# Optimization experiments

Measured on AMD Instinct MI355X. Metric: run time of the kernel, lower is better.

## Reference

```python
import jax, jax.numpy as jnp
from jax import lax
import numpy as np

N_FFT = 1024
HOP = 256
CUTOFF = N_FFT // 2 + 1  # 513


def _make_bases():
    n = np.arange(N_FFT)
    # periodic hann window (scipy get_window('hann', N, fftbins=True))
    win = 0.5 - 0.5 * np.cos(2.0 * np.pi * n / N_FFT)
    fb = np.fft.fft(np.eye(N_FFT))
    FB = np.vstack([fb[:CUTOFF].real, fb[:CUTOFF].imag])  # [1026, 1024]
    scale = N_FFT / HOP
    fwd = (FB * win[None, :]).astype(np.float32)                      # [1026, 1024]
    inv = (np.linalg.pinv(scale * FB).T * win[None, :]).astype(np.float32)  # [1026, 1024]
    win_sq = (win ** 2).astype(np.float32)
    return jnp.asarray(fwd), jnp.asarray(inv), jnp.asarray(win_sq)

FWD_BASIS, INV_BASIS, WIN_SQ = _make_bases()


def setup_inputs() -> dict:
    key = jax.random.key(0)
    k1, k2 = jax.random.split(key)
    audio = jax.random.normal(k1, (4, 1048576), dtype=jnp.float32)
    bias_spec = jax.random.uniform(k2, (1, CUTOFF, 1), dtype=jnp.float32)
    return {"audio": audio, "bias_spec": bias_spec}


def reference(audio, bias_spec):
    strength = 0.1
    pad = N_FFT // 2
    # ---- STFT.transform: reflect pad + strided conv1d with fourier basis ----
    x = jnp.pad(audio, ((0, 0), (pad, pad)), mode='reflect')[:, None, :]  # [B,1,T+N]
    ft = lax.conv_general_dilated(
        x, FWD_BASIS[:, None, :], window_strides=(HOP,), padding='VALID',
        dimension_numbers=('NCH', 'OIH', 'NCH'))  # [B, 1026, F]
    re, im = ft[:, :CUTOFF, :], ft[:, CUTOFF:, :]
    mag = jnp.sqrt(re * re + im * im)
    phase = jnp.arctan2(im, re)
    # ---- denoise: bias subtract + clamp ----
    mag_d = jnp.maximum(mag - bias_spec * strength, 0.0)
    # ---- STFT.inverse: cos/sin recombine + conv_transpose1d ----
    rec = jnp.concatenate([mag_d * jnp.cos(phase), mag_d * jnp.sin(phase)], axis=1)  # [B,1026,F]
    # conv_transpose1d(stride=HOP) == dilated conv with flipped, channel-swapped kernel
    K = jnp.flip(INV_BASIS, axis=-1)[None, :, :]  # OIH: [1, 1026, 1024]
    inv = lax.conv_general_dilated(
        rec, K, window_strides=(1,), padding=[(N_FFT - 1, N_FFT - 1)],
        lhs_dilation=(HOP,), dimension_numbers=('NCH', 'OIH', 'NCH'))  # [B,1,(F-1)*HOP+N]
    # ---- window_sumsquare (vectorized overlap-add of win_sq) ----
    F = mag.shape[-1]
    n_len = N_FFT + HOP * (F - 1)
    idx = (jnp.arange(F)[:, None] * HOP + jnp.arange(N_FFT)[None, :]).reshape(-1)
    ws = jnp.zeros((n_len,), jnp.float32).at[idx].add(jnp.tile(WIN_SQ, F))
    tiny = jnp.finfo(jnp.float32).tiny
    inv = jnp.where(ws > tiny, inv / ws, inv) * (float(N_FFT) / HOP)
    # trim filter_length/2 from both ends
    return inv[:, :, pad:-pad]
```

## Files before the change

### kernel.cpp

```cpp
#include <hip/hip_runtime.h>
#include <math.h>


#define NFFT 1024
#define HOP  256
#define CUT  513
#define NB   4
#define LAUD 1048576
#define NFR  4097
#define NFRP 4224
#define FTROWS 4232
#define ABLEN 1082368

typedef __attribute__((ext_vector_type(4))) float f32x4;
typedef __attribute__((ext_vector_type(8))) short bf16x8;

#define AS1 __attribute__((address_space(1)))
#define AS3 __attribute__((address_space(3)))

__device__ __forceinline__ unsigned short f2bf(float x) {
    unsigned u = __float_as_uint(x);
    u += 0x7FFF + ((u >> 16) & 1);
    return (unsigned short)(u >> 16);
}

__global__ __launch_bounds__(256) void build_bases_k(
    ushort* __restrict__ fwd, ushort* __restrict__ invW) {
    __shared__ float ctab[1024];
    const int tid = threadIdx.x, bx = blockIdx.x;
    const float CST = 6.135923151542565e-3f;
    #pragma unroll
    for (int i = 0; i < 4; ++i) ctab[(i << 8) + tid] = cosf(CST * (float)((i << 8) + tid));
    __syncthreads();
    #pragma unroll
    for (int r = 0; r < 4; ++r) {
        int c = (bx << 2) + r;
        int k = (c < CUT) ? c : (c - 512);
        #pragma unroll
        for (int ch = 0; ch < 4; ++ch) {
            int n = (ch << 8) + tid;
            int m = (k * n) & 1023;
            float base = (c < CUT) ? ctab[m] : -ctab[(m + 768) & 1023];
            float win = 0.5f - 0.5f * ctab[n];
            fwd[(c << 10) + n] = f2bf(base * win);
        }
    }
    #pragma unroll
    for (int r = 0; r < 4; ++r) {
        int n = (bx << 2) + r;
        float win = 0.5f - 0.5f * ctab[n];
        long obase = ((long)(n & 255) << 12) + ((long)(n >> 8) << 10);
        #pragma unroll
        for (int ch = 0; ch < 4; ++ch) {
            int c = (ch << 8) + tid;
            int k = (c < CUT) ? c : (c - 512);
            int m = (k * n) & 1023;
            float base = (c < CUT) ? ctab[m] : -ctab[(m + 768) & 1023];
            float d = (c == 0 || c == 512) ? (1.0f / 1024.0f) : (2.0f / 1024.0f);
            invW[obase + c] = f2bf(0.25f * base * d * win);
        }
    }
}

__global__ void cvt_audio_k(const float* __restrict__ audio,
                            ushort* __restrict__ aud, ushort* __restrict__ ft) {
    const int NV = ABLEN / 8;
    int idx = blockIdx.x * blockDim.x + threadIdx.x;
    if (idx < NB * NV) {
        int b = idx / NV;
        int t8 = (idx - b * NV) << 3;
        const float* ap = audio + (long)b * LAUD;
        ushort o[8];
        int j0 = t8 - 512;
        if (j0 >= 0 && j0 + 7 < LAUD) {
            f32x4 v0 = *(const f32x4*)(ap + j0);
            f32x4 v1 = *(const f32x4*)(ap + j0 + 4);
            #pragma unroll
            for (int q = 0; q < 4; ++q) { o[q] = f2bf(v0[q]); o[4 + q] = f2bf(v1[q]); }
        } else {
            #pragma unroll
            for (int q = 0; q < 8; ++q) {
                int t = t8 + q;
                float v = 0.f;
                if (t < LAUD + 1024) {
                    int j = t - 512;
                    if (j < 0) j = -j;
                    if (j >= LAUD) j = 2 * LAUD - 2 - j;
                    v = ap[j];
                }
                o[q] = f2bf(v);
            }
        }
        *(ushort4*)(aud + (long)b * ABLEN + t8)     = *(ushort4*)&o[0];
        *(ushort4*)(aud + (long)b * ABLEN + t8 + 4) = *(ushort4*)&o[4];
    } else if (idx < NB * NV + 512) {
        int e = idx - NB * NV;
        int b = e >> 7, c8 = (e & 127) << 3;
        ushort z[8] = {};
        *(ushort4*)(ft + (long)b * FTROWS * 1024 + c8)     = *(ushort4*)&z[0];
        *(ushort4*)(ft + (long)b * FTROWS * 1024 + c8 + 4) = *(ushort4*)&z[4];
    }
}

__global__ __launch_bounds__(256) void gemm_fwd_k(
    const ushort* __restrict__ fwd, const ushort* __restrict__ aud,
    const float* __restrict__ bias, ushort* __restrict__ ft) {
    __shared__ char smem[32768];
    const int tid = threadIdx.x;
    const int wid = tid >> 6, lane = tid & 63;
    const int lh = lane & 15, lg = lane >> 4;
    const int wm = wid >> 1, wn = wid & 1;
    int w = (blockIdx.x & 7) * 132 + (blockIdx.x >> 3);
    const int f0 = (w % 33) << 7;
    const int c0 = ((w / 33) & 7) << 6;
    const int b  = w / 264;
    const ushort* ab = aud + (long)b * ABLEN;
    f32x4 acc[4][4] = {};

    for (int k0 = 0; k0 < 1024; k0 += 64) {
        if (k0) __syncthreads();
        #pragma unroll
        for (int i = 0; i < 4; ++i) {
            int ci = (i << 8) + tid;
            int row = ci >> 3;
            int ks = k0 + (((ci & 7) ^ (row & 7)) << 3);
            int grow = ((row >> 4) & 1) * 512 + c0 + ((row >> 5) << 4) + (row & 15);
            __builtin_amdgcn_global_load_lds(
                (const AS1 unsigned int*)(fwd + (grow << 10) + ks),
                (AS3 unsigned int*)(smem + (i << 12) + (wid << 10)), 16, 0, 0);
            __builtin_amdgcn_global_load_lds(
                (const AS1 unsigned int*)(ab + (f0 + row) * HOP + ks),
                (AS3 unsigned int*)(smem + 16384 + (i << 12) + (wid << 10)), 16, 0, 0);
        }
        __syncthreads();
        #pragma unroll
        for (int s = 0; s < 2; ++s) {
            bf16x8 av[4], bv[4];
            #pragma unroll
            for (int i = 0; i < 4; ++i) {
                int r = (wm << 6) + (i << 4) + lh;
                av[i] = *(const bf16x8*)(smem + (r << 7) + ((((s << 2) + lg) ^ (r & 7)) << 4));
                int q = (wn << 6) + (i << 4) + lh;
                bv[i] = *(const bf16x8*)(smem + 16384 + (q << 7) + ((((s << 2) + lg) ^ (q & 7)) << 4));
            }
            #pragma unroll
            for (int i = 0; i < 4; ++i)
                #pragma unroll
                for (int j = 0; j < 4; ++j)
                    acc[i][j] = __builtin_amdgcn_mfma_f32_16x16x32_bf16(av[i], bv[j], acc[i][j], 0, 0, 0);
        }
    }
    ushort* ftb = ft + (long)b * FTROWS * 1024 + 1024;
    float b512 = bias[512] * 0.1f;
    #pragma unroll
    for (int p = 0; p < 2; ++p) {
        int kbase = c0 + ((wm * 2 + p) << 4) + (lg << 2);
        float bs[4];
        #pragma unroll
        for (int q = 0; q < 4; ++q) bs[q] = bias[kbase + q] * 0.1f;
        #pragma unroll
        for (int j = 0; j < 4; ++j) {
            int f = f0 + (wn << 6) + (j << 4) + lh;
            bool valid = (f < NFR);
            ushort4 ore, oim;
            #pragma unroll
            for (int q = 0; q < 4; ++q) {
                float re = acc[2 * p][j][q], im = acc[2 * p + 1][j][q];
                float sre, sim;
                if (kbase + q == 0) {
                    float mre = fabsf(re), mim = fabsf(im);
                    sre = mre > 0.f ? fmaxf(mre - bs[0], 0.f) / mre : 0.f;
                    sim = mim > 0.f ? fmaxf(mim - b512, 0.f) / mim : 0.f;
                } else {
                    float mag = sqrtf(re * re + im * im);
                    float s = mag > 0.f ? fmaxf(mag - bs[q], 0.f) / mag : 0.f;
                    sre = s; sim = s;
                }
                ((unsigned short*)&ore)[q] = f2bf(valid ? re * sre : 0.f);
                ((unsigned short*)&oim)[q] = f2bf(valid ? im * sim : 0.f);
            }
            *(ushort4*)(ftb + ((long)f << 10) + kbase) = ore;
            *(ushort4*)(ftb + ((long)f << 10) + 512 + kbase) = oim;
        }
    }
}

__global__ __launch_bounds__(512) void gemm_ola_k(
    const ushort* __restrict__ invW, const ushort* __restrict__ ft,
    float* __restrict__ out) {
    __shared__ char smem[49152];
    const int tid = threadIdx.x;
    const int wid = tid >> 6, lane = tid & 63;
    const int lh = lane & 15, lg = lane >> 4;
    const int g = wid >> 2;
    const int wid2 = wid & 3;
    const int wm = wid2 >> 1, wn = wid2 & 1;
    const int tg = tid & 255;
    int w = (blockIdx.x & 7) * 64 + (blockIdx.x >> 3);
    const int h0  = (w & 1) << 7;
    const int fo0 = 2 + (((w >> 1) & 63) << 6);
    const int b   = w >> 7;
    const ushort* ftb = ft + (long)b * FTROWS * 1024;
    char* sm = smem + g * 24576;
    f32x4 acc[4][2] = {};

    for (int k0 = 0; k0 < 2048; k0 += 64) {
        if (k0) __syncthreads();
        int kk = (g << 11) + k0;
        int d  = kk >> 10;
        int cb = kk & 1023;
        #pragma unroll
        for (int i = 0; i < 4; ++i) {
            int ci = (i << 8) + tg;
            int row = ci >> 3;
            int swz = (((ci & 7) ^ (row & 7)) << 3);
            __builtin_amdgcn_global_load_lds(
                (const AS1 unsigned int*)(invW + ((h0 + row) << 12) + kk + swz),
                (AS3 unsigned int*)(sm + (i << 12) + (wid2 << 10)), 16, 0, 0);
        }
        #pragma unroll
        for (int i = 0; i < 2; ++i) {
            int ci = (i << 8) + tg;
            int row = ci >> 3;
            int swz = (((ci & 7) ^ (row & 7)) << 3);
            int frow = fo0 + row - d + 1;
            __builtin_amdgcn_global_load_lds(
                (const AS1 unsigned int*)(ftb + ((long)frow << 10) + cb + swz),
                (AS3 unsigned int*)(sm + 16384 + (i << 12) + (wid2 << 10)), 16, 0, 0);
        }
        __syncthreads();
        #pragma unroll
        for (int s = 0; s < 2; ++s) {
            bf16x8 av[4], bv[2];
            #pragma unroll
            for (int i = 0; i < 4; ++i) {
                int r = (wm << 6) + (i << 4) + lh;
                av[i] = *(const bf16x8*)(sm + (r << 7) + ((((s << 2) + lg) ^ (r & 7)) << 4));
            }
            #pragma unroll
            for (int j = 0; j < 2; ++j) {
                int rq = (wn << 5) + (j << 4) + lh;
                bv[j] = *(const bf16x8*)(sm + 16384 + (rq << 7) + ((((s << 2) + lg) ^ (rq & 7)) << 4));
            }
            #pragma unroll
            for (int i = 0; i < 4; ++i)
                #pragma unroll
                for (int j = 0; j < 2; ++j)
                    acc[i][j] = __builtin_amdgcn_mfma_f32_16x16x32_bf16(av[i], bv[j], acc[i][j], 0, 0, 0);
        }
    }
    __syncthreads();
    float* red = (float*)smem;
    if (g == 1) {
        #pragma unroll
        for (int i = 0; i < 4; ++i)
            #pragma unroll
            for (int j = 0; j < 2; ++j) {
                int hl = (wm << 6) + (i << 4) + (lg << 2);
                int fl = (wn << 5) + (j << 4) + lh;
                #pragma unroll
                for (int q = 0; q < 4; ++q)
                    red[(hl + q) * 64 + fl] = acc[i][j][q];
            }
    }
    __syncthreads();
    if (g == 1) return;
    float* ob = out + (long)b * LAUD;
    const float CST = 6.135923151542565e-3f;
    #pragma unroll
    for (int i = 0; i < 4; ++i) {
        int hbase = h0 + (wm << 6) + (i << 4) + (lg << 2);
        int hl = (wm << 6) + (i << 4) + (lg << 2);
        #pragma unroll
        for (int j = 0; j < 2; ++j) {
            int fo = fo0 + (wn << 5) + (j << 4) + lh;
            int fl = (wn << 5) + (j << 4) + lh;
            f32x4 v = acc[i][j];
            #pragma unroll
            for (int q = 0; q < 4; ++q) v[q] += red[(hl + q) * 64 + fl];
            if (fo == 2 || fo == 4097) {
                #pragma unroll
                for (int q = 0; q < 4; ++q) {
                    int n = (fo == 2) ? (hbase + q + 768) : (hbase + q);
                    float w2 = 0.5f - 0.5f * cosf(CST * (float)n);
                    v[q] = v[q] * (4.0f / (1.5f - w2 * w2));
                }
            } else {
                v *= (8.0f / 3.0f);
            }
            *(f32x4*)(ob + (((long)(fo - 2)) << 8) + hbase) = v;
        }
    }
}

extern "C" void kernel_launch(void* const* d_in, const int* in_sizes, int n_in,
                              void* d_out, int out_size, void* d_ws, size_t ws_size,
                              hipStream_t stream) {
    const float* audio = (const float*)d_in[0];
    const float* bias  = (const float*)d_in[1];
    float* out = (float*)d_out;
    char* wsb = (char*)d_ws;

    ushort* fwd  = (ushort*)(wsb);
    ushort* invW = (ushort*)(wsb + 2097152);
    ushort* aud  = (ushort*)(wsb + 4194304);
    ushort* ft   = (ushort*)(wsb + 12853248);

    build_bases_k<<<256, 256, 0, stream>>>(fwd, invW);

    int cvt_total = NB * (ABLEN / 8) + 512;
    cvt_audio_k<<<(cvt_total + 255) / 256, 256, 0, stream>>>(audio, aud, ft);

    gemm_fwd_k<<<1056, 256, 0, stream>>>(fwd, aud, bias, ft);

    gemm_ola_k<<<512, 512, 0, stream>>>(invW, ft, out);
}
```

Baseline: 108.3 us.

## Stage whole audio span in LDS once and double-buffer basis tiles

The forward STFT GEMM now loads the block's full overlapping audio span (about 67KB) into LDS once, with an XOR swizzle, instead of reloading an audio tile every k-step. Because frames overlap by 3/4, this removes redundant global traffic for the audio operand. The basis tiles are double-buffered so the next k-step's load overlaps the current MFMA work, leaving one barrier per iteration. LDS use per block grows from 32KB to about 98KB, which limits occupancy to one block per CU and may reduce latency hiding.

```diff
diff --git a/kernel.cpp b/kernel.cpp
--- a/kernel.cpp
+++ b/kernel.cpp
@@ -105,7 +105,7 @@
 __global__ __launch_bounds__(256) void gemm_fwd_k(
     const ushort* __restrict__ fwd, const ushort* __restrict__ aud,
     const float* __restrict__ bias, ushort* __restrict__ ft) {
-    __shared__ char smem[32768];
+    __shared__ __align__(16) char smem[100352];
     const int tid = threadIdx.x;
     const int wid = tid >> 6, lane = tid & 63;
     const int lh = lane & 15, lg = lane >> 4;
@@ -114,34 +114,59 @@
     const int f0 = (w % 33) << 7;
     const int c0 = ((w / 33) & 7) << 6;
     const int b  = w / 264;
-    const ushort* ab = aud + (long)b * ABLEN;
+    const char* abB = (const char*)(aud + (long)b * ABLEN + f0 * HOP);
     f32x4 acc[4][4] = {};
 
+    #pragma unroll
+    for (int it = 0; it < 17; ++it) {
+        int chunk = (it << 8) + tid;
+        if (chunk < 4192) {
+            int pb = chunk << 4;
+            int src = pb ^ (((pb >> 9) & 7) << 4);
+            __builtin_amdgcn_global_load_lds(
+                (const AS1 unsigned int*)(abB + src),
+                (AS3 unsigned int*)(smem + 32768 + (it << 12) + (wid << 10)),
+                16, 0, 0);
+        }
+    }
+    #pragma unroll
+    for (int i = 0; i < 4; ++i) {
+        int ci = (i << 8) + tid;
+        int row = ci >> 3;
+        int ks = ((ci & 7) ^ (row & 7)) << 3;
+        int grow = ((row >> 4) & 1) * 512 + c0 + ((row >> 5) << 4) + (row & 15);
+        __builtin_amdgcn_global_load_lds(
+            (const AS1 unsigned int*)(fwd + (grow << 10) + ks),
+            (AS3 unsigned int*)(smem + (i << 12) + (wid << 10)), 16, 0, 0);
+    }
+    __syncthreads();
+
     for (int k0 = 0; k0 < 1024; k0 += 64) {
-        if (k0) __syncthreads();
-        #pragma unroll
-        for (int i = 0; i < 4; ++i) {
-            int ci = (i << 8) + tid;
-            int row = ci >> 3;
-            int ks = k0 + (((ci & 7) ^ (row & 7)) << 3);
-            int grow = ((row >> 4) & 1) * 512 + c0 + ((row >> 5) << 4) + (row & 15);
-            __builtin_amdgcn_global_load_lds(
-                (const AS1 unsigned int*)(fwd + (grow << 10) + ks),
-                (AS3 unsigned int*)(smem + (i << 12) + (wid << 10)), 16, 0, 0);
-            __builtin_amdgcn_global_load_lds(
-                (const AS1 unsigned int*)(ab + (f0 + row) * HOP + ks),
-                (AS3 unsigned int*)(smem + 16384 + (i << 12) + (wid << 10)), 16, 0, 0);
-        }
-        __syncthreads();
+        const int cur = (k0 >> 6) & 1;
+        if (k0 < 960) {
+            #pragma unroll
+            for (int i = 0; i < 4; ++i) {
+                int ci = (i << 8) + tid;
+                int row = ci >> 3;
+                int ks = k0 + 64 + (((ci & 7) ^ (row & 7)) << 3);
+                int grow = ((row >> 4) & 1) * 512 + c0 + ((row >> 5) << 4) + (row & 15);
+                __builtin_amdgcn_global_load_lds(
+                    (const AS1 unsigned int*)(fwd + (grow << 10) + ks),
+                    (AS3 unsigned int*)(smem + ((cur ^ 1) << 14) + (i << 12) + (wid << 10)),
+                    16, 0, 0);
+            }
+        }
         #pragma unroll
         for (int s = 0; s < 2; ++s) {
             bf16x8 av[4], bv[4];
             #pragma unroll
             for (int i = 0; i < 4; ++i) {
                 int r = (wm << 6) + (i << 4) + lh;
-                av[i] = *(const bf16x8*)(smem + (r << 7) + ((((s << 2) + lg) ^ (r & 7)) << 4));
+                av[i] = *(const bf16x8*)(smem + (cur << 14) + (r << 7) + ((((s << 2) + lg) ^ (r & 7)) << 4));
                 int q = (wn << 6) + (i << 4) + lh;
-                bv[i] = *(const bf16x8*)(smem + 16384 + (q << 7) + ((((s << 2) + lg) ^ (q & 7)) << 4));
+                int x = (q << 9) + ((k0 + (s << 5) + (lg << 3)) << 1);
+                int p = x ^ (((x >> 9) & 7) << 4);
+                bv[i] = *(const bf16x8*)(smem + 32768 + p);
             }
             #pragma unroll
             for (int i = 0; i < 4; ++i)
@@ -149,6 +174,7 @@
                 for (int j = 0; j < 4; ++j)
                     acc[i][j] = __builtin_amdgcn_mfma_f32_16x16x32_bf16(av[i], bv[j], acc[i][j], 0, 0, 0);
         }
+        __syncthreads();
     }
     ushort* ftb = ft + (long)b * FTROWS * 1024 + 1024;
     float b512 = bias[512] * 0.1f;
```

New measurement: 135.0 us. 1.25x slower.

## Split forward GEMM K dimension across two warp groups with LDS reduction

Applied to the files above, without the earlier changes.

The forward STFT GEMM block grows from 256 to 512 threads. Each group of four waves handles half of the K=1024 reduction in its own 32KB LDS region, and the partial accumulators are then summed through LDS before the epilogue. The goal is more waves per tile to hide latency, since the grid of 1056 blocks is small relative to the CU count. The cost is doubled LDS per block, which can lower occupancy, plus an extra reduction pass with two barriers.

```diff
diff --git a/kernel.cpp b/kernel.cpp
--- a/kernel.cpp
+++ b/kernel.cpp
@@ -102,35 +102,46 @@
     }
 }
 
-__global__ __launch_bounds__(256) void gemm_fwd_k(
+__global__ __launch_bounds__(512) void gemm_fwd_k(
     const ushort* __restrict__ fwd, const ushort* __restrict__ aud,
     const float* __restrict__ bias, ushort* __restrict__ ft) {
-    __shared__ char smem[32768];
+    __shared__ __align__(16) char smem[65536];
     const int tid = threadIdx.x;
     const int wid = tid >> 6, lane = tid & 63;
     const int lh = lane & 15, lg = lane >> 4;
-    const int wm = wid >> 1, wn = wid & 1;
+    const int g = wid >> 2;
+    const int wid2 = wid & 3;
+    const int wm = wid2 >> 1, wn = wid2 & 1;
+    const int tg = tid & 255;
     int w = (blockIdx.x & 7) * 132 + (blockIdx.x >> 3);
     const int f0 = (w % 33) << 7;
     const int c0 = ((w / 33) & 7) << 6;
     const int b  = w / 264;
     const ushort* ab = aud + (long)b * ABLEN;
+    char* sg = smem + g * 32768;
     f32x4 acc[4][4] = {};
 
-    for (int k0 = 0; k0 < 1024; k0 += 64) {
-        if (k0) __syncthreads();
+    for (int k0s = 0; k0s < 512; k0s += 64) {
+        if (k0s) __syncthreads();
+        const int k0 = (g << 9) + k0s;
         #pragma unroll
         for (int i = 0; i < 4; ++i) {
-            int ci = (i << 8) + tid;
+            int ci = (i << 8) + tg;
             int row = ci >> 3;
             int ks = k0 + (((ci & 7) ^ (row & 7)) << 3);
             int grow = ((row >> 4) & 1) * 512 + c0 + ((row >> 5) << 4) + (row & 15);
             __builtin_amdgcn_global_load_lds(
                 (const AS1 unsigned int*)(fwd + (grow << 10) + ks),
-                (AS3 unsigned int*)(smem + (i << 12) + (wid << 10)), 16, 0, 0);
+                (AS3 unsigned int*)(sg + (i << 12) + (wid2 << 10)), 16, 0, 0);
+        }
+        #pragma unroll
+        for (int i = 0; i < 4; ++i) {
+            int ci = (i << 8) + tg;
+            int row = ci >> 3;
+            int ks = k0 + (((ci & 7) ^ (row & 7)) << 3);
             __builtin_amdgcn_global_load_lds(
                 (const AS1 unsigned int*)(ab + (f0 + row) * HOP + ks),
-                (AS3 unsigned int*)(smem + 16384 + (i << 12) + (wid << 10)), 16, 0, 0);
+                (AS3 unsigned int*)(sg + 16384 + (i << 12) + (wid2 << 10)), 16, 0, 0);
         }
         __syncthreads();
         #pragma unroll
@@ -139,9 +150,9 @@
             #pragma unroll
             for (int i = 0; i < 4; ++i) {
                 int r = (wm << 6) + (i << 4) + lh;
-                av[i] = *(const bf16x8*)(smem + (r << 7) + ((((s << 2) + lg) ^ (r & 7)) << 4));
+                av[i] = *(const bf16x8*)(sg + (r << 7) + ((((s << 2) + lg) ^ (r & 7)) << 4));
                 int q = (wn << 6) + (i << 4) + lh;
-                bv[i] = *(const bf16x8*)(smem + 16384 + (q << 7) + ((((s << 2) + lg) ^ (q & 7)) << 4));
+                bv[i] = *(const bf16x8*)(sg + 16384 + (q << 7) + ((((s << 2) + lg) ^ (q & 7)) << 4));
             }
             #pragma unroll
             for (int i = 0; i < 4; ++i)
@@ -150,6 +161,36 @@
                     acc[i][j] = __builtin_amdgcn_mfma_f32_16x16x32_bf16(av[i], bv[j], acc[i][j], 0, 0, 0);
         }
     }
+    __syncthreads();
+    float* red = (float*)smem;
+    if (g == 1) {
+        #pragma unroll
+        for (int i = 0; i < 4; ++i)
+            #pragma unroll
+            for (int j = 0; j < 4; ++j) {
+                int hlb = (wm << 6) + (i << 4) + (lg << 2);
+                int fl  = (wn << 6) + (j << 4) + lh;
+                #pragma unroll
+                for (int q = 0; q < 4; ++q) {
+                    int hl = hlb + q;
+                    red[(hl << 7) + (fl ^ ((hl & 12) << 2))] = acc[i][j][q];
+                }
+            }
+    }
+    __syncthreads();
+    if (g == 1) return;
+    #pragma unroll
+    for (int i = 0; i < 4; ++i)
+        #pragma unroll
+        for (int j = 0; j < 4; ++j) {
+            int hlb = (wm << 6) + (i << 4) + (lg << 2);
+            int fl  = (wn << 6) + (j << 4) + lh;
+            #pragma unroll
+            for (int q = 0; q < 4; ++q) {
+                int hl = hlb + q;
+                acc[i][j][q] += red[(hl << 7) + (fl ^ ((hl & 12) << 2))];
+            }
+        }
     ushort* ftb = ft + (long)b * FTROWS * 1024 + 1024;
     float b512 = bias[512] * 0.1f;
     #pragma unroll
@@ -311,7 +352,7 @@
     int cvt_total = NB * (ABLEN / 8) + 512;
     cvt_audio_k<<<(cvt_total + 255) / 256, 256, 0, stream>>>(audio, aud, ft);
 
-    gemm_fwd_k<<<1056, 256, 0, stream>>>(fwd, aud, bias, ft);
+    gemm_fwd_k<<<1056, 512, 0, stream>>>(fwd, aud, bias, ft);
 
     gemm_ola_k<<<512, 512, 0, stream>>>(invW, ft, out);
 }
```

After: 125.0 us. 15.4% more time.

## Factor STFT GEMMs into 256-point DFT segments with twiddle recombination

Applied to the files above, without the earlier changes.

The forward 1024-point windowed DFT becomes a 256-length-K GEMM over hop-sized segments. The four segment partial DFTs are then combined with quarter-rotation twiddles, and the Hann window is applied in the frequency domain as a 3-tap convolution. The inverse path does the mirror: elementwise kernels pre-combine overlapping frames before a K=1024 GEMM instead of K=4096. This cuts GEMM FLOPs about fourfold, but adds two memory-bound elementwise passes and large intermediate bf16 buffers (T, Z, C), plus extra bf16 rounding steps.

```diff
diff --git a/kernel.cpp b/kernel.cpp
--- a/kernel.cpp
+++ b/kernel.cpp
@@ -8,8 +8,9 @@
 #define NB   4
 #define LAUD 1048576
 #define NFR  4097
-#define NFRP 4224
-#define FTROWS 4232
+#define NSEG 4224
+#define NZROW 4100
+#define NCOL 4096
 #define ABLEN 1082368
 
 typedef __attribute__((ext_vector_type(4))) float f32x4;
@@ -23,88 +24,71 @@
     u += 0x7FFF + ((u >> 16) & 1);
     return (unsigned short)(u >> 16);
 }
+__device__ __forceinline__ float bf2f(unsigned short h) {
+    return __uint_as_float(((unsigned)h) << 16);
+}
 
 __global__ __launch_bounds__(256) void build_bases_k(
-    ushort* __restrict__ fwd, ushort* __restrict__ invW) {
+    ushort* __restrict__ fwdT, ushort* __restrict__ invT2) {
     __shared__ float ctab[1024];
     const int tid = threadIdx.x, bx = blockIdx.x;
     const float CST = 6.135923151542565e-3f;
     #pragma unroll
     for (int i = 0; i < 4; ++i) ctab[(i << 8) + tid] = cosf(CST * (float)((i << 8) + tid));
     __syncthreads();
-    #pragma unroll
-    for (int r = 0; r < 4; ++r) {
-        int c = (bx << 2) + r;
-        int k = (c < CUT) ? c : (c - 512);
-        #pragma unroll
-        for (int ch = 0; ch < 4; ++ch) {
-            int n = (ch << 8) + tid;
-            int m = (k * n) & 1023;
-            float base = (c < CUT) ? ctab[m] : -ctab[(m + 768) & 1023];
-            float win = 0.5f - 0.5f * ctab[n];
-            fwd[(c << 10) + n] = f2bf(base * win);
-        }
-    }
-    #pragma unroll
-    for (int r = 0; r < 4; ++r) {
-        int n = (bx << 2) + r;
-        float win = 0.5f - 0.5f * ctab[n];
-        long obase = ((long)(n & 255) << 12) + ((long)(n >> 8) << 10);
-        #pragma unroll
-        for (int ch = 0; ch < 4; ++ch) {
-            int c = (ch << 8) + tid;
-            int k = (c < CUT) ? c : (c - 512);
-            int m = (k * n) & 1023;
-            float base = (c < CUT) ? ctab[m] : -ctab[(m + 768) & 1023];
-            float d = (c == 0 || c == 512) ? (1.0f / 1024.0f) : (2.0f / 1024.0f);
-            invW[obase + c] = f2bf(0.25f * base * d * win);
-        }
-    }
-}
-
-__global__ void cvt_audio_k(const float* __restrict__ audio,
-                            ushort* __restrict__ aud, ushort* __restrict__ ft) {
+    int idx = (bx << 8) + tid;
+    {
+        int ch = idx >> 8, h = idx & 255;
+        int k = (ch < CUT) ? ch : ch - 512;
+        int m = (k * h) & 1023;
+        float base = (ch < CUT) ? ctab[m] : -ctab[(m + 768) & 1023];
+        fwdT[idx] = f2bf(base);
+    }
+    {
+        int h = idx >> 10, ch = idx & 1023;
+        int k = (ch < CUT) ? ch : ch - 512;
+        int m = (k * h) & 1023;
+        float base = (ch < CUT) ? ctab[m] : -ctab[(m + 768) & 1023];
+        float d = (k == 0 || k == 512) ? (1.0f / 1024.0f) : (2.0f / 1024.0f);
+        invT2[idx] = f2bf(base * d);
+    }
+}
+
+__global__ void cvt_audio_k(const float* __restrict__ audio, ushort* __restrict__ aud) {
     const int NV = ABLEN / 8;
     int idx = blockIdx.x * blockDim.x + threadIdx.x;
-    if (idx < NB * NV) {
-        int b = idx / NV;
-        int t8 = (idx - b * NV) << 3;
-        const float* ap = audio + (long)b * LAUD;
-        ushort o[8];
-        int j0 = t8 - 512;
-        if (j0 >= 0 && j0 + 7 < LAUD) {
-            f32x4 v0 = *(const f32x4*)(ap + j0);
-            f32x4 v1 = *(const f32x4*)(ap + j0 + 4);
-            #pragma unroll
-            for (int q = 0; q < 4; ++q) { o[q] = f2bf(v0[q]); o[4 + q] = f2bf(v1[q]); }
-        } else {
-            #pragma unroll
-            for (int q = 0; q < 8; ++q) {
-                int t = t8 + q;
-                float v = 0.f;
-                if (t < LAUD + 1024) {
-                    int j = t - 512;
-                    if (j < 0) j = -j;
-                    if (j >= LAUD) j = 2 * LAUD - 2 - j;
-                    v = ap[j];
-                }
-                o[q] = f2bf(v);
-            }
-        }
-        *(ushort4*)(aud + (long)b * ABLEN + t8)     = *(ushort4*)&o[0];
-        *(ushort4*)(aud + (long)b * ABLEN + t8 + 4) = *(ushort4*)&o[4];
-    } else if (idx < NB * NV + 512) {
-        int e = idx - NB * NV;
-        int b = e >> 7, c8 = (e & 127) << 3;
-        ushort z[8] = {};
-        *(ushort4*)(ft + (long)b * FTROWS * 1024 + c8)     = *(ushort4*)&z[0];
-        *(ushort4*)(ft + (long)b * FTROWS * 1024 + c8 + 4) = *(ushort4*)&z[4];
-    }
-}
-
-__global__ __launch_bounds__(256) void gemm_fwd_k(
-    const ushort* __restrict__ fwd, const ushort* __restrict__ aud,
-    const float* __restrict__ bias, ushort* __restrict__ ft) {
+    if (idx >= NB * NV) return;
+    int b = idx / NV;
+    int t8 = (idx - b * NV) << 3;
+    const float* ap = audio + (long)b * LAUD;
+    ushort o[8];
+    int j0 = t8 - 512;
+    if (j0 >= 0 && j0 + 7 < LAUD) {
+        f32x4 v0 = *(const f32x4*)(ap + j0);
+        f32x4 v1 = *(const f32x4*)(ap + j0 + 4);
+        #pragma unroll
+        for (int q = 0; q < 4; ++q) { o[q] = f2bf(v0[q]); o[4 + q] = f2bf(v1[q]); }
+    } else {
+        #pragma unroll
+        for (int q = 0; q < 8; ++q) {
+            int t = t8 + q;
+            float v = 0.f;
+            if (t < LAUD + 1024) {
+                int j = t - 512;
+                if (j < 0) j = -j;
+                if (j >= LAUD) j = 2 * LAUD - 2 - j;
+                v = ap[j];
+            }
+            o[q] = f2bf(v);
+        }
+    }
+    *(ushort4*)(aud + (long)b * ABLEN + t8)     = *(ushort4*)&o[0];
+    *(ushort4*)(aud + (long)b * ABLEN + t8 + 4) = *(ushort4*)&o[4];
+}
+
+__global__ __launch_bounds__(256) void gemm_t_k(
+    const ushort* __restrict__ fwdT, const ushort* __restrict__ aud,
+    ushort* __restrict__ T) {
     __shared__ char smem[32768];
     const int tid = threadIdx.x;
     const int wid = tid >> 6, lane = tid & 63;
@@ -112,24 +96,23 @@
     const int wm = wid >> 1, wn = wid & 1;
     int w = (blockIdx.x & 7) * 132 + (blockIdx.x >> 3);
     const int f0 = (w % 33) << 7;
-    const int c0 = ((w / 33) & 7) << 6;
+    const int c0 = ((w / 33) & 7) << 7;
     const int b  = w / 264;
     const ushort* ab = aud + (long)b * ABLEN;
     f32x4 acc[4][4] = {};
 
-    for (int k0 = 0; k0 < 1024; k0 += 64) {
+    for (int k0 = 0; k0 < 256; k0 += 64) {
         if (k0) __syncthreads();
         #pragma unroll
         for (int i = 0; i < 4; ++i) {
             int ci = (i << 8) + tid;
             int row = ci >> 3;
             int ks = k0 + (((ci & 7) ^ (row & 7)) << 3);
-            int grow = ((row >> 4) & 1) * 512 + c0 + ((row >> 5) << 4) + (row & 15);
             __builtin_amdgcn_global_load_lds(
-                (const AS1 unsigned int*)(fwd + (grow << 10) + ks),
+                (const AS1 unsigned int*)(fwdT + ((c0 + row) << 8) + ks),
                 (AS3 unsigned int*)(smem + (i << 12) + (wid << 10)), 16, 0, 0);
             __builtin_amdgcn_global_load_lds(
-                (const AS1 unsigned int*)(ab + (f0 + row) * HOP + ks),
+                (const AS1 unsigned int*)(ab + (f0 + row) * 256 + ks),
                 (AS3 unsigned int*)(smem + 16384 + (i << 12) + (wid << 10)), 16, 0, 0);
         }
         __syncthreads();
@@ -150,43 +133,117 @@
                     acc[i][j] = __builtin_amdgcn_mfma_f32_16x16x32_bf16(av[i], bv[j], acc[i][j], 0, 0, 0);
         }
     }
-    ushort* ftb = ft + (long)b * FTROWS * 1024 + 1024;
-    float b512 = bias[512] * 0.1f;
-    #pragma unroll
-    for (int p = 0; p < 2; ++p) {
-        int kbase = c0 + ((wm * 2 + p) << 4) + (lg << 2);
-        float bs[4];
-        #pragma unroll
-        for (int q = 0; q < 4; ++q) bs[q] = bias[kbase + q] * 0.1f;
+    ushort* Tb = T + (long)b * NSEG * 1024;
+    #pragma unroll
+    for (int i = 0; i < 4; ++i) {
+        int c = c0 + (wm << 6) + (i << 4) + (lg << 2);
         #pragma unroll
         for (int j = 0; j < 4; ++j) {
-            int f = f0 + (wn << 6) + (j << 4) + lh;
-            bool valid = (f < NFR);
-            ushort4 ore, oim;
-            #pragma unroll
-            for (int q = 0; q < 4; ++q) {
-                float re = acc[2 * p][j][q], im = acc[2 * p + 1][j][q];
-                float sre, sim;
-                if (kbase + q == 0) {
-                    float mre = fabsf(re), mim = fabsf(im);
-                    sre = mre > 0.f ? fmaxf(mre - bs[0], 0.f) / mre : 0.f;
-                    sim = mim > 0.f ? fmaxf(mim - b512, 0.f) / mim : 0.f;
-                } else {
-                    float mag = sqrtf(re * re + im * im);
-                    float s = mag > 0.f ? fmaxf(mag - bs[q], 0.f) / mag : 0.f;
-                    sre = s; sim = s;
-                }
-                ((unsigned short*)&ore)[q] = f2bf(valid ? re * sre : 0.f);
-                ((unsigned short*)&oim)[q] = f2bf(valid ? im * sim : 0.f);
-            }
-            *(ushort4*)(ftb + ((long)f << 10) + kbase) = ore;
-            *(ushort4*)(ftb + ((long)f << 10) + 512 + kbase) = oim;
-        }
-    }
-}
-
-__global__ __launch_bounds__(512) void gemm_ola_k(
-    const ushort* __restrict__ invW, const ushort* __restrict__ ft,
+            int g = f0 + (wn << 6) + (j << 4) + lh;
+            ushort4 o;
+            o.x = f2bf(acc[i][j][0]); o.y = f2bf(acc[i][j][1]);
+            o.z = f2bf(acc[i][j][2]); o.w = f2bf(acc[i][j][3]);
+            *(ushort4*)(Tb + ((long)g << 10) + c) = o;
+        }
+    }
+}
+
+__device__ __forceinline__ float2 combineX(const ushort* __restrict__ Tr, int m) {
+    bool cj = false;
+    if (m < 0) { m = -m; cj = true; }
+    else if (m > 512) { m = 1024 - m; cj = true; }
+    float a[4], bb[4];
+    #pragma unroll
+    for (int d = 0; d < 4; ++d) {
+        a[d]  = bf2f(Tr[(d << 10) + m]);
+        bb[d] = (m >= 1 && m <= 511) ? bf2f(Tr[(d << 10) + 512 + m]) : 0.f;
+    }
+    int r = m & 3;
+    float xr, xi;
+    if      (r == 0) { xr = a[0] + a[1] + a[2] + a[3];   xi = bb[0] + bb[1] + bb[2] + bb[3]; }
+    else if (r == 1) { xr = a[0] + bb[1] - a[2] - bb[3]; xi = bb[0] - a[1] - bb[2] + a[3]; }
+    else if (r == 2) { xr = a[0] - a[1] + a[2] - a[3];   xi = bb[0] - bb[1] + bb[2] - bb[3]; }
+    else             { xr = a[0] - bb[1] - a[2] + bb[3]; xi = bb[0] + a[1] - bb[2] - a[3]; }
+    float2 res; res.x = xr; res.y = cj ? -xi : xi;
+    return res;
+}
+
+__device__ __forceinline__ void nonlin_store(const ushort* Tr, const float* bias,
+                                             ushort* Zr, int k) {
+    float2 xm = combineX(Tr, k - 1);
+    float2 x0 = combineX(Tr, k);
+    float2 xp = combineX(Tr, k + 1);
+    float xwr = 0.5f * x0.x - 0.25f * (xm.x + xp.x);
+    float xwi = 0.5f * x0.y - 0.25f * (xm.y + xp.y);
+    float mag = sqrtf(xwr * xwr + xwi * xwi);
+    float s = mag > 0.f ? fmaxf(mag - 0.1f * bias[k], 0.f) / mag : 0.f;
+    Zr[k] = f2bf(xwr * s);
+    if (k >= 1 && k <= 511) Zr[512 + k] = f2bf(xwi * s);
+}
+
+__global__ __launch_bounds__(256) void elem_a_k(
+    const ushort* __restrict__ T, const float* __restrict__ bias,
+    ushort* __restrict__ Z) {
+    int bid = blockIdx.x;
+    int b = bid / NFR, f = bid - b * NFR;
+    const ushort* Tr = T + ((long)(b * NSEG + f) << 10);
+    ushort* Zr = Z + ((long)(b * NZROW + f) << 10);
+    int tid = threadIdx.x;
+    nonlin_store(Tr, bias, Zr, tid);
+    nonlin_store(Tr, bias, Zr, tid + 256);
+    if (tid == 0) nonlin_store(Tr, bias, Zr, 512);
+}
+
+__device__ __forceinline__ float2 loadZ(const ushort* __restrict__ Zr, int m) {
+    bool cj = false;
+    if (m < 0) { m = -m; cj = true; }
+    else if (m > 512) { m = 1024 - m; cj = true; }
+    float zr = bf2f(Zr[m]);
+    float zi = (m >= 1 && m <= 511) ? bf2f(Zr[512 + m]) : 0.f;
+    float2 res; res.x = zr; res.y = cj ? -zi : zi;
+    return res;
+}
+
+__device__ __forceinline__ void comb_store(const ushort* Zb, ushort* Cr, int g, int k) {
+    int r = k & 3;
+    float cr = 0.f, ci = 0.f;
+    #pragma unroll
+    for (int d = 0; d < 4; ++d) {
+        int f = g - d;
+        if (f < 0 || f >= NFR) continue;
+        const ushort* Zr = Zb + ((long)f << 10);
+        float2 zm = loadZ(Zr, k - 1);
+        float2 z0 = loadZ(Zr, k);
+        float2 zp = loadZ(Zr, k + 1);
+        float ar = 0.5f * z0.x - 0.25f * (zm.x + zp.x);
+        float ai = 0.5f * z0.y - 0.25f * (zm.y + zp.y);
+        int rd = (d * r) & 3;
+        float er, ei;
+        if      (rd == 0) { er = ar;  ei = ai; }
+        else if (rd == 1) { er = -ai; ei = ar; }
+        else if (rd == 2) { er = -ar; ei = -ai; }
+        else              { er = ai;  ei = -ar; }
+        cr += er; ci += ei;
+    }
+    Cr[k] = f2bf(cr);
+    if (k >= 1 && k <= 511) Cr[512 + k] = f2bf(ci);
+}
+
+__global__ __launch_bounds__(256) void elem_b_k(
+    const ushort* __restrict__ Z, ushort* __restrict__ C) {
+    int bid = blockIdx.x;
+    int b = bid >> 12, j = bid & 4095;
+    int g = j + 2;
+    const ushort* Zb = Z + (long)b * NZROW * 1024;
+    ushort* Cr = C + ((long)(b * NCOL + j) << 10);
+    int tid = threadIdx.x;
+    comb_store(Zb, Cr, g, tid);
+    comb_store(Zb, Cr, g, tid + 256);
+    if (tid == 0) comb_store(Zb, Cr, g, 512);
+}
+
+__global__ __launch_bounds__(512) void gemm_c_k(
+    const ushort* __restrict__ invT2, const ushort* __restrict__ C,
     float* __restrict__ out) {
     __shared__ char smem[49152];
     const int tid = threadIdx.x;
@@ -198,24 +255,23 @@
     const int tg = tid & 255;
     int w = (blockIdx.x & 7) * 64 + (blockIdx.x >> 3);
     const int h0  = (w & 1) << 7;
-    const int fo0 = 2 + (((w >> 1) & 63) << 6);
+    const int j0  = ((w >> 1) & 63) << 6;
+    const int fo0 = 2 + j0;
     const int b   = w >> 7;
-    const ushort* ftb = ft + (long)b * FTROWS * 1024;
+    const ushort* Cb = C + (long)b * NCOL * 1024;
     char* sm = smem + g * 24576;
     f32x4 acc[4][2] = {};
 
-    for (int k0 = 0; k0 < 2048; k0 += 64) {
-        if (k0) __syncthreads();
-        int kk = (g << 11) + k0;
-        int d  = kk >> 10;
-        int cb = kk & 1023;
+    for (int k0s = 0; k0s < 512; k0s += 64) {
+        if (k0s) __syncthreads();
+        int kk = (g << 9) + k0s;
         #pragma unroll
         for (int i = 0; i < 4; ++i) {
             int ci = (i << 8) + tg;
             int row = ci >> 3;
             int swz = (((ci & 7) ^ (row & 7)) << 3);
             __builtin_amdgcn_global_load_lds(
-                (const AS1 unsigned int*)(invW + ((h0 + row) << 12) + kk + swz),
+                (const AS1 unsigned int*)(invT2 + ((h0 + row) << 10) + kk + swz),
                 (AS3 unsigned int*)(sm + (i << 12) + (wid2 << 10)), 16, 0, 0);
         }
         #pragma unroll
@@ -223,9 +279,8 @@
             int ci = (i << 8) + tg;
             int row = ci >> 3;
             int swz = (((ci & 7) ^ (row & 7)) << 3);
-            int frow = fo0 + row - d + 1;
             __builtin_amdgcn_global_load_lds(
-                (const AS1 unsigned int*)(ftb + ((long)frow << 10) + cb + swz),
+                (const AS1 unsigned int*)(Cb + ((long)(j0 + row) << 10) + kk + swz),
                 (AS3 unsigned int*)(sm + 16384 + (i << 12) + (wid2 << 10)), 16, 0, 0);
         }
         __syncthreads();
@@ -283,10 +338,10 @@
                 for (int q = 0; q < 4; ++q) {
                     int n = (fo == 2) ? (hbase + q + 768) : (hbase + q);
                     float w2 = 0.5f - 0.5f * cosf(CST * (float)n);
-                    v[q] = v[q] * (4.0f / (1.5f - w2 * w2));
+                    v[q] = v[q] * (1.0f / (1.5f - w2 * w2));
                 }
             } else {
-                v *= (8.0f / 3.0f);
+                v *= (2.0f / 3.0f);
             }
             *(f32x4*)(ob + (((long)(fo - 2)) << 8) + hbase) = v;
         }
@@ -301,17 +356,23 @@
     float* out = (float*)d_out;
     char* wsb = (char*)d_ws;
 
-    ushort* fwd  = (ushort*)(wsb);
-    ushort* invW = (ushort*)(wsb + 2097152);
-    ushort* aud  = (ushort*)(wsb + 4194304);
-    ushort* ft   = (ushort*)(wsb + 12853248);
-
-    build_bases_k<<<256, 256, 0, stream>>>(fwd, invW);
-
-    int cvt_total = NB * (ABLEN / 8) + 512;
-    cvt_audio_k<<<(cvt_total + 255) / 256, 256, 0, stream>>>(audio, aud, ft);
-
-    gemm_fwd_k<<<1056, 256, 0, stream>>>(fwd, aud, bias, ft);
-
-    gemm_ola_k<<<512, 512, 0, stream>>>(invW, ft, out);
-}
+    ushort* fwdT  = (ushort*)(wsb);
+    ushort* invT2 = (ushort*)(wsb + 524288);
+    ushort* aud   = (ushort*)(wsb + 1048576);
+    ushort* T     = (ushort*)(wsb + 9707520);
+    ushort* Z     = (ushort*)(wsb + 44310528);
+    ushort* C     = (ushort*)(wsb + 77897728);
+
+    build_bases_k<<<1024, 256, 0, stream>>>(fwdT, invT2);
+
+    int cvt_total = NB * (ABLEN / 8);
+    cvt_audio_k<<<(cvt_total + 255) / 256, 256, 0, stream>>>(audio, aud);
+
+    gemm_t_k<<<1056, 256, 0, stream>>>(fwdT, aud, T);
+
+    elem_a_k<<<NB * NFR, 256, 0, stream>>>(T, bias, Z);
+
+    elem_b_k<<<NB * NCOL, 256, 0, stream>>>(Z, C);
+
+    gemm_c_k<<<512, 512, 0, stream>>>(invT2, C, out);
+}
```

New measurement: 200.1 us. 1.85x slower.
